# Kernel tuning notes

Measured on AMD Instinct MI355X. Metric: run time of the kernel, lower is better.

The kernel has to match this reference:

```python
import jax, jax.numpy as jnp
import numpy as np

D_MODEL = 1024
H = 16
D_K = 64
D_V = 64
D_G = D_MODEL // H  # 64, trignometric embedding
WAVE_LEN = 1000.0
B = 8
N = 512


def box_relational_embedding(boxes, dim_g=D_G):
    # boxes: (b, n, 4) as (x_min, y_min, x_max, y_max)
    x_min, y_min, x_max, y_max = jnp.split(boxes, 4, axis=-1)  # each (b, n, 1)
    cx = (x_min + x_max) * 0.5
    cy = (y_min + y_max) * 0.5
    w = (x_max - x_min) + 1.0
    h = (y_max - y_min) + 1.0
    # pairwise log-ratios, (b, n, n)
    delta_x = jnp.log(jnp.clip(jnp.abs((cx - jnp.swapaxes(cx, 1, 2)) / w), 1e-3, None))
    delta_y = jnp.log(jnp.clip(jnp.abs((cy - jnp.swapaxes(cy, 1, 2)) / h), 1e-3, None))
    delta_w = jnp.log(w / jnp.swapaxes(w, 1, 2))
    delta_h = jnp.log(h / jnp.swapaxes(h, 1, 2))
    pos = jnp.stack([delta_x, delta_y, delta_w, delta_h], axis=-1)  # (b, n, n, 4)
    n_freq = dim_g // 8
    feat_range = jnp.arange(n_freq, dtype=jnp.float32)
    dim_mat = 1.0 / (WAVE_LEN ** (feat_range / n_freq))  # (n_freq,)
    mul = (100.0 * pos)[..., None] * dim_mat  # (b, n, n, 4, n_freq)
    b, n = pos.shape[0], pos.shape[1]
    mul = mul.reshape(b, n, n, 4 * n_freq)
    return jnp.concatenate([jnp.sin(mul), jnp.cos(mul)], axis=-1)  # (b, n, n, dim_g)


def setup_inputs() -> dict:
    key = jax.random.key(0)
    ks = jax.random.split(key, 12)
    s = 0.02
    inp = {
        "queries": jax.random.normal(ks[0], (B, N, D_MODEL), jnp.float32),
        "keys": jax.random.normal(ks[1], (B, N, D_MODEL), jnp.float32),
        "values": jax.random.normal(ks[2], (B, N, D_MODEL), jnp.float32),
        "boxes": jax.random.uniform(ks[3], (B, N, 4), jnp.float32),
        "Wq": jax.random.normal(ks[4], (H * D_K, D_MODEL), jnp.float32) * s,
        "bq": jnp.zeros((H * D_K,), jnp.float32),
        "Wk": jax.random.normal(ks[5], (H * D_K, D_MODEL), jnp.float32) * s,
        "bk": jnp.zeros((H * D_K,), jnp.float32),
        "Wv": jax.random.normal(ks[6], (H * D_V, D_MODEL), jnp.float32) * s,
        "bv": jnp.zeros((H * D_V,), jnp.float32),
        "Wo": jax.random.normal(ks[7], (D_MODEL, H * D_V), jnp.float32) * s,
        "bo": jnp.zeros((D_MODEL,), jnp.float32),
        "Wg": jax.random.normal(ks[8], (H, D_G), jnp.float32) * s,  # h separate Linear(d_g,1) stacked
        "bg": jnp.zeros((H,), jnp.float32),
    }
    return inp


def reference(queries, keys, values, boxes, Wq, bq, Wk, bk, Wv, bv, Wo, bo, Wg, bg):
    b, nq, _ = queries.shape
    nk = keys.shape[1]
    # per-head geometry bias
    emb = box_relational_embedding(boxes)  # (b, nk, nk, D_G)
    g = jax.nn.relu(jnp.einsum('bnmd,hd->bhnm', emb, Wg) + bg[None, :, None, None])
    # QKV projections, split heads
    q = (queries @ Wq.T + bq).reshape(b, nq, H, D_K).transpose(0, 2, 1, 3)  # (b,h,nq,dk)
    k = (keys @ Wk.T + bk).reshape(b, nk, H, D_K).transpose(0, 2, 1, 3)    # (b,h,nk,dk)
    v = (values @ Wv.T + bv).reshape(b, nk, H, D_V).transpose(0, 2, 1, 3)  # (b,h,nk,dv)
    a = jnp.einsum('bhqd,bhkd->bhqk', q, k) / jnp.sqrt(jnp.float32(D_K))
    mn = jax.nn.softmax(jnp.log(jnp.clip(g, 1e-6, None)) + a, axis=-1)
    out = jnp.einsum('bhqk,bhkd->bqhd', mn, v).reshape(b, nq, H * D_V)
    return out @ Wo.T + bo
```

## Files before the change

### kernel.cpp

```cpp
#include <hip/hip_runtime.h>
#include <hip/hip_bf16.h>
#include <hip/hip_fp16.h>

typedef __attribute__((ext_vector_type(8))) short bf16x8;
typedef __attribute__((ext_vector_type(8))) _Float16 f16x8;
typedef __attribute__((ext_vector_type(4))) float f32x4;
typedef __attribute__((ext_vector_type(8))) short short8;

__device__ __forceinline__ short f2bf(float x) {
    unsigned u = __builtin_bit_cast(unsigned, x);
    u += 0x7fffu + ((u >> 16) & 1u);
    return (short)(u >> 16);
}

__device__ __forceinline__ void load_lds16(const void* g, void* l) {
    __builtin_amdgcn_global_load_lds((const __attribute__((address_space(1))) unsigned int*)g,
                                     (__attribute__((address_space(3))) unsigned int*)l, 16, 0, 0);
}

__global__ void convert_qkv(const float* __restrict__ q, const float* __restrict__ k,
                            const float* __restrict__ v, short* __restrict__ qo,
                            short* __restrict__ ko, short* __restrict__ vo) {
    int i = blockIdx.x * 256 + threadIdx.x;
    const float* s = blockIdx.y == 0 ? q : blockIdx.y == 1 ? k : v;
    short* d = blockIdx.y == 0 ? qo : blockIdx.y == 1 ? ko : vo;
    float4 val = reinterpret_cast<const float4*>(s)[i];
    short4 o; o.x = f2bf(val.x); o.y = f2bf(val.y); o.z = f2bf(val.z); o.w = f2bf(val.w);
    reinterpret_cast<short4*>(d)[i] = o;
}

__global__ void convert_w4(const float* __restrict__ w0, const float* __restrict__ w1,
                           const float* __restrict__ w2, const float* __restrict__ w3,
                           short* __restrict__ o0, short* __restrict__ o1,
                           short* __restrict__ o2, short* __restrict__ o3) {
    int i = blockIdx.x * 256 + threadIdx.x;
    const float* s = blockIdx.y == 0 ? w0 : blockIdx.y == 1 ? w1 : blockIdx.y == 2 ? w2 : w3;
    short* d = blockIdx.y == 0 ? o0 : blockIdx.y == 1 ? o1 : blockIdx.y == 2 ? o2 : o3;
    float4 val = reinterpret_cast<const float4*>(s)[i];
    short4 o; o.x = f2bf(val.x); o.y = f2bf(val.y); o.z = f2bf(val.z); o.w = f2bf(val.w);
    reinterpret_cast<short4*>(d)[i] = o;
}

__global__ void convert_f32_f16(const float* __restrict__ src, _Float16* __restrict__ dst, int n) {
    int i = blockIdx.x * blockDim.x + threadIdx.x;
    if (i < n) dst[i] = (_Float16)src[i];
}

__global__ void geom_kernel3(const float* __restrict__ boxes, const _Float16* __restrict__ Wgh,
                             const float* __restrict__ bg, __half* __restrict__ G) {
    const int tid = threadIdx.x;
    const int wave = tid >> 6, lane = tid & 63, quad = lane >> 4, l16 = lane & 15;
    const int m0 = blockIdx.x * 64;
    const int n = blockIdx.y;
    const int b = blockIdx.z;

    __shared__ __align__(16) _Float16 feat[4][16][72];
    __shared__ __align__(16) _Float16 gbuf[16][68];

    const int p = lane >> 2, c = lane & 3;
    const int m = m0 + wave * 16 + p;

    float4 bn = reinterpret_cast<const float4*>(boxes)[b * 512 + n];
    float4 bm = reinterpret_cast<const float4*>(boxes)[b * 512 + m];
    float cxn = (bn.x + bn.z) * 0.5f, cyn = (bn.y + bn.w) * 0.5f;
    float wn = bn.z - bn.x + 1.0f, hn = bn.w - bn.y + 1.0f;
    float cxm = (bm.x + bm.z) * 0.5f, cym = (bm.y + bm.w) * 0.5f;
    float wm = bm.z - bm.x + 1.0f, hm = bm.w - bm.y + 1.0f;

    float num = (c == 0) ? fabsf(cxn - cxm) : (c == 1) ? fabsf(cyn - cym) : (c == 2) ? wn : hn;
    float den = (c == 0) ? wn : (c == 1) ? hn : (c == 2) ? wm : hm;
    float lr = __logf(num) - __logf(den);
    if (c < 2) lr = fmaxf(lr, -6.9077552790f);
    float pos = lr * 100.0f;

    const float dm[8] = {1.0f, 0.42169651f, 0.17782794f, 0.07498942f,
                         0.03162278f, 0.01333521f, 0.00562341f, 0.00237137f};
    f16x8 sv8, cv8;
    #pragma unroll
    for (int f = 0; f < 8; ++f) {
        float th = pos * dm[f];
        sv8[f] = (_Float16)__sinf(th);
        cv8[f] = (_Float16)__cosf(th);
    }
    *(f16x8*)&feat[wave][p][c * 8]      = sv8;
    *(f16x8*)&feat[wave][p][32 + c * 8] = cv8;

    __syncthreads();

    f16x8 a0 = *(const f16x8*)&feat[wave][l16][quad * 8];
    f16x8 a1 = *(const f16x8*)&feat[wave][l16][32 + quad * 8];
    f16x8 b0 = *(const f16x8*)(Wgh + l16 * 64 + quad * 8);
    f16x8 b1 = *(const f16x8*)(Wgh + l16 * 64 + 32 + quad * 8);
    f32x4 acc = (f32x4){0.f, 0.f, 0.f, 0.f};
    acc = __builtin_amdgcn_mfma_f32_16x16x32_f16(a0, b0, acc, 0, 0, 0);
    acc = __builtin_amdgcn_mfma_f32_16x16x32_f16(a1, b1, acc, 0, 0, 0);

    float bgv = bg[l16];
    #pragma unroll
    for (int rr = 0; rr < 4; ++rr) {
        float g = fmaxf(acc[rr] + bgv, 1e-6f);
        gbuf[l16][wave * 16 + quad * 4 + rr] = (_Float16)g;
    }
    __syncthreads();

    const int h = tid >> 4, seg = tid & 15;
    ushort4 v = *(const ushort4*)&gbuf[h][seg * 4];
    *(ushort4*)&G[((long)((b * 16 + h) * 512 + n)) * 512 + m0 + seg * 4] = v;
}

#define PROJ_COMP(BC)                                                                  \
    {                                                                                  \
        bf16x8 a_[4], bb_[4];                                                          \
        _Pragma("unroll")                                                              \
        for (int g = 0; g < 4; ++g)                                                    \
            a_[g] = *(const bf16x8*)&As[BC][(wr * 64 + g * 16 + l16) * 32 + quad * 8]; \
        _Pragma("unroll")                                                              \
        for (int g = 0; g < 4; ++g)                                                    \
            bb_[g] = *(const bf16x8*)&Bs[BC][(wc * 64 + g * 16 + l16) * 32 + quad * 8];\
        _Pragma("unroll")                                                              \
        for (int mg = 0; mg < 4; ++mg)                                                 \
            _Pragma("unroll")                                                          \
            for (int ng = 0; ng < 4; ++ng)                                             \
                acc[mg][ng] = __builtin_amdgcn_mfma_f32_16x16x32_bf16(a_[mg], bb_[ng], acc[mg][ng], 0, 0, 0); \
    }

#define PROJ_STEP(T, BC, BS)                                                           \
    {                                                                                  \
        asm volatile("s_waitcnt vmcnt(4)" ::: "memory");                               \
        __builtin_amdgcn_s_barrier();                                                  \
        const int k1_ = ((T) + 2) * 32;                                                \
        load_lds16(ga0 + k1_, &As[BS][wb]);                                            \
        load_lds16(ga1 + k1_, &As[BS][2048 + wb]);                                     \
        load_lds16(gb0 + k1_, &Bs[BS][wb]);                                            \
        load_lds16(gb1 + k1_, &Bs[BS][2048 + wb]);                                     \
        PROJ_COMP(BC)                                                                  \
    }

__global__ __launch_bounds__(256, 3)
void proj_all4(const short* __restrict__ qkbf, const short* __restrict__ wqkb,
               const short* __restrict__ wvb, const short* __restrict__ vbf,
               const float* __restrict__ bq, const float* __restrict__ bk,
               const float* __restrict__ bv,
               short* __restrict__ QKh, _Float16* __restrict__ Vt) {
    __shared__ __align__(16) short As[3][4096];
    __shared__ __align__(16) short Bs[3][4096];
    const int tid = threadIdx.x;
    const int wave = tid >> 6, lane = tid & 63, quad = lane >> 4, l16 = lane & 15;
    const int bid = blockIdx.x;

    const short *Ap, *Bp;
    int m0, n0, z = 0;
    bool isV = bid >= 512;
    if (!isV) {
        z = bid >> 8;
        int t = bid & 255;
        n0 = (t & 7) * 128; m0 = (t >> 3) * 128;
        Ap = qkbf + (long)z * 4194304 + (long)m0 * 1024;
        Bp = wqkb + (long)z * 1048576 + (long)n0 * 1024;
    } else {
        int t = bid - 512;
        n0 = (t & 31) * 128; m0 = (t >> 5) * 128;
        Ap = wvb + (long)m0 * 1024;
        Bp = vbf + (long)n0 * 1024;
    }

    f32x4 acc[4][4];
    #pragma unroll
    for (int mg = 0; mg < 4; ++mg)
        #pragma unroll
        for (int ng = 0; ng < 4; ++ng) acc[mg][ng] = (f32x4){0.f, 0.f, 0.f, 0.f};

    const int r0 = tid >> 2, kk = (tid & 3) * 8;
    const short* ga0 = Ap + (long)r0 * 1024 + kk;
    const short* ga1 = Ap + (long)(64 + r0) * 1024 + kk;
    const short* gb0 = Bp + (long)r0 * 1024 + kk;
    const short* gb1 = Bp + (long)(64 + r0) * 1024 + kk;
    const int wb = wave * 512;
    const int wr = wave >> 1, wc = wave & 1;

    load_lds16(ga0, &As[0][wb]);
    load_lds16(ga1, &As[0][2048 + wb]);
    load_lds16(gb0, &Bs[0][wb]);
    load_lds16(gb1, &Bs[0][2048 + wb]);
    load_lds16(ga0 + 32, &As[1][wb]);
    load_lds16(ga1 + 32, &As[1][2048 + wb]);
    load_lds16(gb0 + 32, &Bs[1][wb]);
    load_lds16(gb1 + 32, &Bs[1][2048 + wb]);

    for (int tb = 0; tb < 30; tb += 3) {
        PROJ_STEP(tb,     0, 2)
        PROJ_STEP(tb + 1, 1, 0)
        PROJ_STEP(tb + 2, 2, 1)
    }
    asm volatile("s_waitcnt vmcnt(4)" ::: "memory");
    __builtin_amdgcn_s_barrier();
    PROJ_COMP(0)
    asm volatile("s_waitcnt vmcnt(0)" ::: "memory");
    __builtin_amdgcn_s_barrier();
    PROJ_COMP(1)

    #pragma unroll
    for (int mg = 0; mg < 4; ++mg)
        #pragma unroll
        for (int ng = 0; ng < 4; ++ng)
            #pragma unroll
            for (int r = 0; r < 4; ++r) {
                int row = m0 + wr * 64 + mg * 16 + quad * 4 + r;
                int col = n0 + wc * 64 + ng * 16 + l16;
                if (!isV) {
                    float v = acc[mg][ng][r] + (z ? bk[col] : bq[col]);
                    QKh[(long)z * 4194304 + (long)row * 1024 + col] = f2bf(v);
                } else {
                    float v = acc[mg][ng][r] + bv[row];
                    int bcol = col >> 9, lc = col & 511;
                    Vt[(long)bcol * 524288 + (long)row * 512 + lc] = (_Float16)v;
                }
            }
}

__global__ __launch_bounds__(256, 4)
void flash_attn6(const short* __restrict__ Q, const short* __restrict__ Kh,
                 const _Float16* __restrict__ Vt, const __half* __restrict__ G,
                 short* __restrict__ O) {
    const int tid = threadIdx.x;
    const int wave = tid >> 6, lane = tid & 63, quad = lane >> 4, l16 = lane & 15;
    const int qt = blockIdx.x, h = blockIdx.y, b = blockIdx.z;

    __shared__ __align__(16) short    Ks[64][72];
    __shared__ __align__(16) _Float16 Vs[64][72];
    __shared__ __align__(16) _Float16 Gs[64][72];
    __shared__ __align__(16) _Float16 Pbuf[4][16][72];

    const int qrow = qt * 64 + wave * 16;
    const long qoff = ((long)(b * 512 + qrow + l16)) * 1024 + h * 64 + quad * 8;
    bf16x8 aq0 = *(const bf16x8*)(Q + qoff);
    bf16x8 aq1 = *(const bf16x8*)(Q + qoff + 32);

    const int sr0 = tid >> 3,         sc0 = (tid & 7) * 8;
    const int sr1 = (tid + 256) >> 3, sc1 = ((tid + 256) & 7) * 8;
    const short* Kbase = Kh + (long)(b * 512) * 1024 + h * 64;
    const _Float16* Vbase = Vt + (long)b * 524288 + (long)(h * 64) * 512;
    const _Float16* Gbase = (const _Float16*)G + ((long)((b * 16 + h) * 512 + qt * 64)) * 512;

    f32x4 oacc[4];
    #pragma unroll
    for (int r = 0; r < 4; ++r) oacc[r] = (f32x4){0.f, 0.f, 0.f, 0.f};
    float rs = 0.f;

    for (int kt = 0; kt < 8; ++kt) {
        __syncthreads();
        short8 k0 = *(const short8*)(Kbase + (long)(kt * 64 + sr0) * 1024 + sc0);
        short8 k1 = *(const short8*)(Kbase + (long)(kt * 64 + sr1) * 1024 + sc1);
        short8 v0 = *(const short8*)(Vbase + (long)sr0 * 512 + kt * 64 + sc0);
        short8 v1 = *(const short8*)(Vbase + (long)sr1 * 512 + kt * 64 + sc1);
        short8 g0 = *(const short8*)(Gbase + (long)sr0 * 512 + kt * 64 + sc0);
        short8 g1 = *(const short8*)(Gbase + (long)sr1 * 512 + kt * 64 + sc1);
        *(short8*)&Ks[sr0][sc0] = k0;
        *(short8*)&Ks[sr1][sc1] = k1;
        *(short8*)&Vs[sr0][sc0] = v0;
        *(short8*)&Vs[sr1][sc1] = v1;
        *(short8*)&Gs[sr0][sc0] = g0;
        *(short8*)&Gs[sr1][sc1] = g1;
        __syncthreads();

        f32x4 sc[4];
        #pragma unroll
        for (int nk = 0; nk < 4; ++nk) {
            bf16x8 bk0 = *(const bf16x8*)&Ks[nk * 16 + l16][quad * 8];
            bf16x8 bk1 = *(const bf16x8*)&Ks[nk * 16 + l16][32 + quad * 8];
            f32x4 s = (f32x4){0.f, 0.f, 0.f, 0.f};
            s = __builtin_amdgcn_mfma_f32_16x16x32_bf16(aq0, bk0, s, 0, 0, 0);
            s = __builtin_amdgcn_mfma_f32_16x16x32_bf16(aq1, bk1, s, 0, 0, 0);
            sc[nk] = s;
        }
        #pragma unroll
        for (int nk = 0; nk < 4; ++nk)
            #pragma unroll
            for (int r = 0; r < 4; ++r)
                Pbuf[wave][quad * 4 + r][nk * 16 + l16] = (_Float16)__expf(sc[nk][r] * 0.125f);
        f16x8 ep0 = *(const f16x8*)&Pbuf[wave][l16][quad * 8];
        f16x8 ep1 = *(const f16x8*)&Pbuf[wave][l16][32 + quad * 8];
        f16x8 gA = *(const f16x8*)&Gs[wave * 16 + l16][quad * 8];
        f16x8 gB = *(const f16x8*)&Gs[wave * 16 + l16][32 + quad * 8];
        f16x8 gp0 = ep0 * gA;
        f16x8 gp1 = ep1 * gB;
        float part = 0.f;
        #pragma unroll
        for (int j = 0; j < 8; ++j) part += (float)gp0[j] + (float)gp1[j];
        rs += part;
        #pragma unroll
        for (int n4 = 0; n4 < 4; ++n4) {
            f16x8 bv0 = *(const f16x8*)&Vs[n4 * 16 + l16][quad * 8];
            f16x8 bv1 = *(const f16x8*)&Vs[n4 * 16 + l16][32 + quad * 8];
            oacc[n4] = __builtin_amdgcn_mfma_f32_16x16x32_f16(gp0, bv0, oacc[n4], 0, 0, 0);
            oacc[n4] = __builtin_amdgcn_mfma_f32_16x16x32_f16(gp1, bv1, oacc[n4], 0, 0, 0);
        }
    }

    rs += __shfl_xor(rs, 16);
    rs += __shfl_xor(rs, 32);
    float li[4];
    #pragma unroll
    for (int r = 0; r < 4; ++r) li[r] = __shfl(rs, quad * 4 + r);

    #pragma unroll
    for (int n4 = 0; n4 < 4; ++n4)
        #pragma unroll
        for (int r = 0; r < 4; ++r) {
            float o = oacc[n4][r] / li[r];
            O[((long)(b * 512 + qrow + quad * 4 + r)) * 1024 + h * 64 + n4 * 16 + l16] = f2bf(o);
        }
}

#define GOUT_COMP(BC)                                                                  \
    {                                                                                  \
        bf16x8 a_[2], bb_[4];                                                          \
        _Pragma("unroll")                                                              \
        for (int g = 0; g < 2; ++g)                                                    \
            a_[g] = *(const bf16x8*)&As[BC][(mw + g * 16 + l16) * 32 + quad * 8];      \
        _Pragma("unroll")                                                              \
        for (int g = 0; g < 4; ++g)                                                    \
            bb_[g] = *(const bf16x8*)&Bs[BC][(g * 16 + l16) * 32 + quad * 8];          \
        _Pragma("unroll")                                                              \
        for (int mg = 0; mg < 2; ++mg)                                                 \
            _Pragma("unroll")                                                          \
            for (int ng = 0; ng < 4; ++ng)                                             \
                acc[mg][ng] = __builtin_amdgcn_mfma_f32_16x16x32_bf16(a_[mg], bb_[ng], acc[mg][ng], 0, 0, 0); \
    }

#define GOUT_STEP(T, BC, BS)                                                           \
    {                                                                                  \
        asm volatile("s_waitcnt vmcnt(3)" ::: "memory");                               \
        __builtin_amdgcn_s_barrier();                                                  \
        const int k1_ = ((T) + 2) * 32;                                                \
        load_lds16(ga0 + k1_, &As[BS][wb]);                                            \
        load_lds16(ga1 + k1_, &As[BS][2048 + wb]);                                     \
        load_lds16(gb0 + k1_, &Bs[BS][wb]);                                            \
        GOUT_COMP(BC)                                                                  \
    }

__global__ __launch_bounds__(256, 4)
void gemm_out3(const short* __restrict__ Hd, const short* __restrict__ wob,
               const float* __restrict__ bo, float* __restrict__ out) {
    __shared__ __align__(16) short As[3][4096];
    __shared__ __align__(16) short Bs[3][2048];
    const int tid = threadIdx.x;
    const int wave = tid >> 6, lane = tid & 63, quad = lane >> 4, l16 = lane & 15;
    const int m0 = blockIdx.y * 128, n0 = blockIdx.x * 64;
    const short* Ap = Hd + (long)m0 * 1024;
    const short* Bp = wob + (long)n0 * 1024;

    f32x4 acc[2][4];
    #pragma unroll
    for (int mg = 0; mg < 2; ++mg)
        #pragma unroll
        for (int ng = 0; ng < 4; ++ng) acc[mg][ng] = (f32x4){0.f, 0.f, 0.f, 0.f};

    const int r0 = tid >> 2, kk = (tid & 3) * 8;
    const short* ga0 = Ap + (long)r0 * 1024 + kk;
    const short* ga1 = Ap + (long)(64 + r0) * 1024 + kk;
    const short* gb0 = Bp + (long)r0 * 1024 + kk;
    const int wb = wave * 512;
    const int mw = wave * 32;

    load_lds16(ga0, &As[0][wb]);
    load_lds16(ga1, &As[0][2048 + wb]);
    load_lds16(gb0, &Bs[0][wb]);
    load_lds16(ga0 + 32, &As[1][wb]);
    load_lds16(ga1 + 32, &As[1][2048 + wb]);
    load_lds16(gb0 + 32, &Bs[1][wb]);

    for (int tb = 0; tb < 30; tb += 3) {
        GOUT_STEP(tb,     0, 2)
        GOUT_STEP(tb + 1, 1, 0)
        GOUT_STEP(tb + 2, 2, 1)
    }
    asm volatile("s_waitcnt vmcnt(3)" ::: "memory");
    __builtin_amdgcn_s_barrier();
    GOUT_COMP(0)
    asm volatile("s_waitcnt vmcnt(0)" ::: "memory");
    __builtin_amdgcn_s_barrier();
    GOUT_COMP(1)

    #pragma unroll
    for (int mg = 0; mg < 2; ++mg)
        #pragma unroll
        for (int ng = 0; ng < 4; ++ng)
            #pragma unroll
            for (int r = 0; r < 4; ++r) {
                int row = m0 + mw + mg * 16 + quad * 4 + r;
                int col = n0 + ng * 16 + l16;
                out[(long)row * 1024 + col] = acc[mg][ng][r] + bo[col];
            }
}

extern "C" void kernel_launch(void* const* d_in, const int* in_sizes, int n_in,
                              void* d_out, int out_size, void* d_ws, size_t ws_size,
                              hipStream_t stream) {
    const float* queries = (const float*)d_in[0];
    const float* keys    = (const float*)d_in[1];
    const float* values  = (const float*)d_in[2];
    const float* boxes   = (const float*)d_in[3];
    const float* bq = (const float*)d_in[5];
    const float* bk = (const float*)d_in[7];
    const float* bv = (const float*)d_in[9];
    const float* bo = (const float*)d_in[11];
    const float* Wg = (const float*)d_in[12];
    const float* bg = (const float*)d_in[13];

    char* ws = (char*)d_ws;
    short* qbf = (short*)(ws + 0);
    short* kbf = (short*)(ws + 8388608);
    short* vbf = (short*)(ws + 16777216);
    short* wqb = (short*)(ws + 25165824);
    short* wkb = (short*)(ws + 27262976);
    short* wvb = (short*)(ws + 29360128);
    short* wob = (short*)(ws + 31457280);
    short* Qh  = (short*)(ws + 33554432);
    _Float16* Vt = (_Float16*)(ws + 50331648);
    short* Hd  = (short*)(ws + 58720256);
    __half* G  = (__half*)(ws + 67108864);
    _Float16* Wgh = (_Float16*)(ws + 33554432);

    convert_qkv<<<dim3(4096, 3), 256, 0, stream>>>(queries, keys, values, qbf, kbf, vbf);
    convert_w4<<<dim3(1024, 4), 256, 0, stream>>>((const float*)d_in[4], (const float*)d_in[6],
                                                  (const float*)d_in[8], (const float*)d_in[10],
                                                  wqb, wkb, wvb, wob);
    convert_f32_f16<<<4, 256, 0, stream>>>(Wg, Wgh, 1024);

    geom_kernel3<<<dim3(8, 512, 8), 256, 0, stream>>>(boxes, Wgh, bg, G);

    proj_all4<<<768, 256, 0, stream>>>(qbf, wqb, wvb, vbf, bq, bk, bv, Qh, Vt);

    flash_attn6<<<dim3(8, 16, 8), 256, 0, stream>>>(Qh, Qh + 4194304, Vt, G, Hd);

    gemm_out3<<<dim3(16, 32), 256, 0, stream>>>(Hd, wob, bo, (float*)d_out);
}
```

Baseline: 269.5 us.

## Batch geometry rows per block and remap GEMM block order for XCD locality

The geometry kernel now handles 8 query rows per block instead of one. This amortises the loads of the m-box, its log widths and heights, Wg and bg, and cuts the grid eightfold; the log ratios for width and height are rewritten as differences of precomputed logs. The projection and output GEMMs remap their block indices so that consecutive blocks dispatched to the same XCD share A/B tiles, aiming for better L2 reuse. The V-projection tile order is also swapped. Fewer geometry blocks and extra barriers per block could reduce latency hiding.

```diff
diff --git a/kernel.cpp b/kernel.cpp
--- a/kernel.cpp
+++ b/kernel.cpp
@@ -46,12 +46,13 @@
     if (i < n) dst[i] = (_Float16)src[i];
 }
 
-__global__ void geom_kernel3(const float* __restrict__ boxes, const _Float16* __restrict__ Wgh,
-                             const float* __restrict__ bg, __half* __restrict__ G) {
+__global__ __launch_bounds__(256)
+void geom_kernel4(const float* __restrict__ boxes, const _Float16* __restrict__ Wgh,
+                  const float* __restrict__ bg, __half* __restrict__ G) {
     const int tid = threadIdx.x;
     const int wave = tid >> 6, lane = tid & 63, quad = lane >> 4, l16 = lane & 15;
     const int m0 = blockIdx.x * 64;
-    const int n = blockIdx.y;
+    const int n0 = blockIdx.y * 8;
     const int b = blockIdx.z;
 
     __shared__ __align__(16) _Float16 feat[4][16][72];
@@ -60,52 +61,59 @@
     const int p = lane >> 2, c = lane & 3;
     const int m = m0 + wave * 16 + p;
 
-    float4 bn = reinterpret_cast<const float4*>(boxes)[b * 512 + n];
     float4 bm = reinterpret_cast<const float4*>(boxes)[b * 512 + m];
-    float cxn = (bn.x + bn.z) * 0.5f, cyn = (bn.y + bn.w) * 0.5f;
-    float wn = bn.z - bn.x + 1.0f, hn = bn.w - bn.y + 1.0f;
     float cxm = (bm.x + bm.z) * 0.5f, cym = (bm.y + bm.w) * 0.5f;
     float wm = bm.z - bm.x + 1.0f, hm = bm.w - bm.y + 1.0f;
-
-    float num = (c == 0) ? fabsf(cxn - cxm) : (c == 1) ? fabsf(cyn - cym) : (c == 2) ? wn : hn;
-    float den = (c == 0) ? wn : (c == 1) ? hn : (c == 2) ? wm : hm;
-    float lr = __logf(num) - __logf(den);
-    if (c < 2) lr = fmaxf(lr, -6.9077552790f);
-    float pos = lr * 100.0f;
+    float lwm = __logf(wm), lhm = __logf(hm);
+
+    f16x8 wb0 = *(const f16x8*)(Wgh + l16 * 64 + quad * 8);
+    f16x8 wb1 = *(const f16x8*)(Wgh + l16 * 64 + 32 + quad * 8);
+    float bgv = bg[l16];
 
     const float dm[8] = {1.0f, 0.42169651f, 0.17782794f, 0.07498942f,
                          0.03162278f, 0.01333521f, 0.00562341f, 0.00237137f};
-    f16x8 sv8, cv8;
-    #pragma unroll
-    for (int f = 0; f < 8; ++f) {
-        float th = pos * dm[f];
-        sv8[f] = (_Float16)__sinf(th);
-        cv8[f] = (_Float16)__cosf(th);
-    }
-    *(f16x8*)&feat[wave][p][c * 8]      = sv8;
-    *(f16x8*)&feat[wave][p][32 + c * 8] = cv8;
-
-    __syncthreads();
-
-    f16x8 a0 = *(const f16x8*)&feat[wave][l16][quad * 8];
-    f16x8 a1 = *(const f16x8*)&feat[wave][l16][32 + quad * 8];
-    f16x8 b0 = *(const f16x8*)(Wgh + l16 * 64 + quad * 8);
-    f16x8 b1 = *(const f16x8*)(Wgh + l16 * 64 + 32 + quad * 8);
-    f32x4 acc = (f32x4){0.f, 0.f, 0.f, 0.f};
-    acc = __builtin_amdgcn_mfma_f32_16x16x32_f16(a0, b0, acc, 0, 0, 0);
-    acc = __builtin_amdgcn_mfma_f32_16x16x32_f16(a1, b1, acc, 0, 0, 0);
-
-    float bgv = bg[l16];
-    #pragma unroll
-    for (int rr = 0; rr < 4; ++rr) {
-        float g = fmaxf(acc[rr] + bgv, 1e-6f);
-        gbuf[l16][wave * 16 + quad * 4 + rr] = (_Float16)g;
-    }
-    __syncthreads();
-
     const int h = tid >> 4, seg = tid & 15;
-    ushort4 v = *(const ushort4*)&gbuf[h][seg * 4];
-    *(ushort4*)&G[((long)((b * 16 + h) * 512 + n)) * 512 + m0 + seg * 4] = v;
+
+    for (int ni = 0; ni < 8; ++ni) {
+        const int n = n0 + ni;
+        float4 bn = reinterpret_cast<const float4*>(boxes)[b * 512 + n];
+        float cxn = (bn.x + bn.z) * 0.5f, cyn = (bn.y + bn.w) * 0.5f;
+        float wn = bn.z - bn.x + 1.0f, hn = bn.w - bn.y + 1.0f;
+        float lwn = __logf(wn), lhn = __logf(hn);
+
+        float numa = (c == 1) ? fabsf(cyn - cym) : fabsf(cxn - cxm);
+        float pl = fmaxf(__logf(numa) - ((c == 1) ? lhn : lwn), -6.9077552790f);
+        float sl = (c == 3) ? (lhn - lhm) : (lwn - lwm);
+        float pos = ((c < 2) ? pl : sl) * 100.0f;
+
+        f16x8 sv8, cv8;
+        #pragma unroll
+        for (int f = 0; f < 8; ++f) {
+            float th = pos * dm[f];
+            sv8[f] = (_Float16)__sinf(th);
+            cv8[f] = (_Float16)__cosf(th);
+        }
+        *(f16x8*)&feat[wave][p][c * 8]      = sv8;
+        *(f16x8*)&feat[wave][p][32 + c * 8] = cv8;
+
+        __syncthreads();
+
+        f16x8 a0 = *(const f16x8*)&feat[wave][l16][quad * 8];
+        f16x8 a1 = *(const f16x8*)&feat[wave][l16][32 + quad * 8];
+        f32x4 acc = (f32x4){0.f, 0.f, 0.f, 0.f};
+        acc = __builtin_amdgcn_mfma_f32_16x16x32_f16(a0, wb0, acc, 0, 0, 0);
+        acc = __builtin_amdgcn_mfma_f32_16x16x32_f16(a1, wb1, acc, 0, 0, 0);
+
+        #pragma unroll
+        for (int rr = 0; rr < 4; ++rr) {
+            float g = fmaxf(acc[rr] + bgv, 1e-6f);
+            gbuf[l16][wave * 16 + quad * 4 + rr] = (_Float16)g;
+        }
+        __syncthreads();
+
+        ushort4 v = *(const ushort4*)&gbuf[h][seg * 4];
+        *(ushort4*)&G[((long)((b * 16 + h) * 512 + n)) * 512 + m0 + seg * 4] = v;
+    }
 }
 
 #define PROJ_COMP(BC)                                                                  \
@@ -137,7 +145,7 @@
     }
 
 __global__ __launch_bounds__(256, 3)
-void proj_all4(const short* __restrict__ qkbf, const short* __restrict__ wqkb,
+void proj_all5(const short* __restrict__ qkbf, const short* __restrict__ wqkb,
                const short* __restrict__ wvb, const short* __restrict__ vbf,
                const float* __restrict__ bq, const float* __restrict__ bk,
                const float* __restrict__ bv,
@@ -146,7 +154,7 @@
     __shared__ __align__(16) short Bs[3][4096];
     const int tid = threadIdx.x;
     const int wave = tid >> 6, lane = tid & 63, quad = lane >> 4, l16 = lane & 15;
-    const int bid = blockIdx.x;
+    const int bid = (blockIdx.x & 7) * 96 + (blockIdx.x >> 3);
 
     const short *Ap, *Bp;
     int m0, n0, z = 0;
@@ -159,7 +167,7 @@
         Bp = wqkb + (long)z * 1048576 + (long)n0 * 1024;
     } else {
         int t = bid - 512;
-        n0 = (t & 31) * 128; m0 = (t >> 5) * 128;
+        m0 = (t & 7) * 128; n0 = (t >> 3) * 128;
         Ap = wvb + (long)m0 * 1024;
         Bp = vbf + (long)n0 * 1024;
     }
@@ -346,7 +354,8 @@
     __shared__ __align__(16) short Bs[3][2048];
     const int tid = threadIdx.x;
     const int wave = tid >> 6, lane = tid & 63, quad = lane >> 4, l16 = lane & 15;
-    const int m0 = blockIdx.y * 128, n0 = blockIdx.x * 64;
+    const int bid = (blockIdx.x & 7) * 64 + (blockIdx.x >> 3);
+    const int m0 = (bid >> 4) * 128, n0 = (bid & 15) * 64;
     const short* Ap = Hd + (long)m0 * 1024;
     const short* Bp = wob + (long)n0 * 1024;
 
@@ -428,11 +437,11 @@
                                                   wqb, wkb, wvb, wob);
     convert_f32_f16<<<4, 256, 0, stream>>>(Wg, Wgh, 1024);
 
-    geom_kernel3<<<dim3(8, 512, 8), 256, 0, stream>>>(boxes, Wgh, bg, G);
-
-    proj_all4<<<768, 256, 0, stream>>>(qbf, wqb, wvb, vbf, bq, bk, bv, Qh, Vt);
+    geom_kernel4<<<dim3(8, 64, 8), 256, 0, stream>>>(boxes, Wgh, bg, G);
+
+    proj_all5<<<768, 256, 0, stream>>>(qbf, wqb, wvb, vbf, bq, bk, bv, Qh, Vt);
 
     flash_attn6<<<dim3(8, 16, 8), 256, 0, stream>>>(Qh, Qh + 4194304, Vt, G, Hd);
 
-    gemm_out3<<<dim3(16, 32), 256, 0, stream>>>(Hd, wob, bo, (float*)d_out);
-}
+    gemm_out3<<<512, 256, 0, stream>>>(Hd, wob, bo, (float*)d_out);
+}
```

Measured after the change: 259.0 us. 3.9% less time.
